# Kernel tuning notes

Hardware: AMD Instinct MI355X
Metric: run time of the kernel (lower is better)

Reference implementation:

```python
import jax, jax.numpy as jnp
import numpy as np

DIM = 300

def setup_inputs() -> dict:
    key = jax.random.key(0)
    k1, k2 = jax.random.split(key)
    article_concat = jax.random.normal(k1, (256, 2048, DIM), dtype=jnp.float32)
    options_concat = jax.random.normal(k2, (256, 64, DIM), dtype=jnp.float32)
    return {"article_concat": article_concat, "options_concat": options_concat}

def reference(article_concat, options_concat):
    # Mean-pool over the word dimension for both inputs, then concat features.
    article_mean = jnp.mean(article_concat, axis=1)   # [B, DIM]
    options_mean = jnp.mean(options_concat, axis=1)   # [B, DIM]
    return jnp.concatenate([article_mean, options_mean], axis=1)  # [B, 2*DIM]
```

## Files before the change

### kernel.cpp

```cpp
#include <hip/hip_runtime.h>


typedef float f4 __attribute__((ext_vector_type(4)));

#define B        256
#define DIM      300
#define J4       75
#define W_ART    2048
#define W_OPT    64
#define SPLIT    8
#define ROWS_PB  (W_ART / SPLIT)
#define ITERS    (ROWS_PB * J4 / DIM)

__global__ __launch_bounds__(DIM) void art_partial_kernel(
    const f4* __restrict__ art,
    f4* __restrict__ part)
{
    const int b = blockIdx.x;
    const int y = blockIdx.y;
    const int t = threadIdx.x;
    const int j = t % J4;

    const f4* p = art + (size_t)b * (W_ART * J4) + (size_t)y * (ROWS_PB * J4) + t;

    f4 a0 = {0.f, 0.f, 0.f, 0.f};
    f4 a1 = {0.f, 0.f, 0.f, 0.f};
    f4 a2 = {0.f, 0.f, 0.f, 0.f};
    f4 a3 = {0.f, 0.f, 0.f, 0.f};
    #pragma unroll 4
    for (int it = 0; it < ITERS; it += 4, p += 4 * DIM) {
        const f4 v0 = __builtin_nontemporal_load(&p[0 * DIM]);
        const f4 v1 = __builtin_nontemporal_load(&p[1 * DIM]);
        const f4 v2 = __builtin_nontemporal_load(&p[2 * DIM]);
        const f4 v3 = __builtin_nontemporal_load(&p[3 * DIM]);
        a0 += v0;
        a1 += v1;
        a2 += v2;
        a3 += v3;
    }
    a0 += a1;
    a2 += a3;
    a0 += a2;

    __shared__ f4 lds[DIM];
    lds[t] = a0;
    __syncthreads();
    if (t < J4) {
        const f4 r = lds[t] + lds[t + J4] + lds[t + 2 * J4] + lds[t + 3 * J4];
        part[((size_t)y * B + b) * J4 + j] = r;
    }
}

__global__ __launch_bounds__(DIM) void finalize_kernel(
    const float* __restrict__ part,
    const float* __restrict__ opt,
    float* __restrict__ out)
{
    const int b = blockIdx.x;
    const int c = threadIdx.x;

    float s = 0.f;
    #pragma unroll
    for (int y = 0; y < SPLIT; ++y)
        s += part[((size_t)y * B + b) * DIM + c];

    const float* ob = opt + (size_t)b * (W_OPT * DIM) + c;
    float o0 = 0.f, o1 = 0.f, o2 = 0.f, o3 = 0.f;
    #pragma unroll 4
    for (int w = 0; w < W_OPT; w += 4) {
        o0 += __builtin_nontemporal_load(&ob[(size_t)(w + 0) * DIM]);
        o1 += __builtin_nontemporal_load(&ob[(size_t)(w + 1) * DIM]);
        o2 += __builtin_nontemporal_load(&ob[(size_t)(w + 2) * DIM]);
        o3 += __builtin_nontemporal_load(&ob[(size_t)(w + 3) * DIM]);
    }

    float* ou = out + (size_t)b * (2 * DIM);
    ou[c]       = s * (1.0f / (float)W_ART);
    ou[DIM + c] = ((o0 + o1) + (o2 + o3)) * (1.0f / (float)W_OPT);
}

extern "C" void kernel_launch(void* const* d_in, const int* in_sizes, int n_in,
                              void* d_out, int out_size, void* d_ws, size_t ws_size,
                              hipStream_t stream) {
    const f4* art = (const f4*)d_in[0];
    const float* opt = (const float*)d_in[1];
    float* out = (float*)d_out;
    f4* part = (f4*)d_ws;

    art_partial_kernel<<<dim3(B, SPLIT), dim3(DIM), 0, stream>>>(art, part);
    finalize_kernel<<<dim3(B), dim3(DIM), 0, stream>>>((const float*)part, opt, out);
}
```

Before: 762.9 us.

## Fuse article and options mean into one kernel without split reduction

Replaces the two-kernel scheme (split partial sums over 8 blocks per batch, then a finalize kernel) with a single kernel of 600 threads per batch row that streams the whole article and options slabs and reduces through shared memory. This removes the second launch and the workspace round-trip, and drops the nontemporal load hints. The trade-off is fewer blocks (256 instead of 2048), which may limit memory-level parallelism on a 256-CU device.

```diff
diff --git a/kernel.cpp b/kernel.cpp
--- a/kernel.cpp
+++ b/kernel.cpp
@@ -8,85 +8,76 @@
 #define J4       75
 #define W_ART    2048
 #define W_OPT    64
-#define SPLIT    8
-#define ROWS_PB  (W_ART / SPLIT)
-#define ITERS    (ROWS_PB * J4 / DIM)
+#define THR      600
+#define GRP      (THR / J4)
+#define ART_F4   (W_ART * J4)
+#define ART_IT   (ART_F4 / THR)
+#define OPT_F4   (W_OPT * J4)
+#define OPT_IT   (OPT_F4 / THR)
 
-__global__ __launch_bounds__(DIM) void art_partial_kernel(
+__global__ __launch_bounds__(THR) void fused_mean_kernel(
     const f4* __restrict__ art,
-    f4* __restrict__ part)
+    const f4* __restrict__ opt,
+    f4* __restrict__ out)
 {
     const int b = blockIdx.x;
-    const int y = blockIdx.y;
     const int t = threadIdx.x;
-    const int j = t % J4;
 
-    const f4* p = art + (size_t)b * (W_ART * J4) + (size_t)y * (ROWS_PB * J4) + t;
-
+    const f4* pa = art + (size_t)b * ART_F4 + t;
     f4 a0 = {0.f, 0.f, 0.f, 0.f};
     f4 a1 = {0.f, 0.f, 0.f, 0.f};
     f4 a2 = {0.f, 0.f, 0.f, 0.f};
     f4 a3 = {0.f, 0.f, 0.f, 0.f};
     #pragma unroll 4
-    for (int it = 0; it < ITERS; it += 4, p += 4 * DIM) {
-        const f4 v0 = __builtin_nontemporal_load(&p[0 * DIM]);
-        const f4 v1 = __builtin_nontemporal_load(&p[1 * DIM]);
-        const f4 v2 = __builtin_nontemporal_load(&p[2 * DIM]);
-        const f4 v3 = __builtin_nontemporal_load(&p[3 * DIM]);
+    for (int it = 0; it < ART_IT; it += 4, pa += 4 * THR) {
+        const f4 v0 = pa[0 * THR];
+        const f4 v1 = pa[1 * THR];
+        const f4 v2 = pa[2 * THR];
+        const f4 v3 = pa[3 * THR];
         a0 += v0;
         a1 += v1;
         a2 += v2;
         a3 += v3;
     }
-    a0 += a1;
-    a2 += a3;
-    a0 += a2;
+    a0 += a1; a2 += a3; a0 += a2;
 
-    __shared__ f4 lds[DIM];
-    lds[t] = a0;
+    const f4* po = opt + (size_t)b * OPT_F4 + t;
+    f4 o0 = {0.f, 0.f, 0.f, 0.f};
+    f4 o1 = {0.f, 0.f, 0.f, 0.f};
+    #pragma unroll
+    for (int it = 0; it < OPT_IT; it += 2, po += 2 * THR) {
+        o0 += po[0];
+        o1 += po[THR];
+    }
+    o0 += o1;
+
+    __shared__ f4 lart[THR];
+    __shared__ f4 lopt[THR];
+    lart[t] = a0;
+    lopt[t] = o0;
     __syncthreads();
+
     if (t < J4) {
-        const f4 r = lds[t] + lds[t + J4] + lds[t + 2 * J4] + lds[t + 3 * J4];
-        part[((size_t)y * B + b) * J4 + j] = r;
+        f4 sa = lart[t];
+        f4 so = lopt[t];
+        #pragma unroll
+        for (int g = 1; g < GRP; ++g) {
+            sa += lart[t + g * J4];
+            so += lopt[t + g * J4];
+        }
+        f4* ou = out + (size_t)b * (2 * J4);
+        ou[t]      = sa * (1.0f / (float)W_ART);
+        ou[J4 + t] = so * (1.0f / (float)W_OPT);
     }
-}
-
-__global__ __launch_bounds__(DIM) void finalize_kernel(
-    const float* __restrict__ part,
-    const float* __restrict__ opt,
-    float* __restrict__ out)
-{
-    const int b = blockIdx.x;
-    const int c = threadIdx.x;
-
-    float s = 0.f;
-    #pragma unroll
-    for (int y = 0; y < SPLIT; ++y)
-        s += part[((size_t)y * B + b) * DIM + c];
-
-    const float* ob = opt + (size_t)b * (W_OPT * DIM) + c;
-    float o0 = 0.f, o1 = 0.f, o2 = 0.f, o3 = 0.f;
-    #pragma unroll 4
-    for (int w = 0; w < W_OPT; w += 4) {
-        o0 += __builtin_nontemporal_load(&ob[(size_t)(w + 0) * DIM]);
-        o1 += __builtin_nontemporal_load(&ob[(size_t)(w + 1) * DIM]);
-        o2 += __builtin_nontemporal_load(&ob[(size_t)(w + 2) * DIM]);
-        o3 += __builtin_nontemporal_load(&ob[(size_t)(w + 3) * DIM]);
-    }
-
-    float* ou = out + (size_t)b * (2 * DIM);
-    ou[c]       = s * (1.0f / (float)W_ART);
-    ou[DIM + c] = ((o0 + o1) + (o2 + o3)) * (1.0f / (float)W_OPT);
 }
 
 extern "C" void kernel_launch(void* const* d_in, const int* in_sizes, int n_in,
                               void* d_out, int out_size, void* d_ws, size_t ws_size,
                               hipStream_t stream) {
     const f4* art = (const f4*)d_in[0];
-    const float* opt = (const float*)d_in[1];
-    float* out = (float*)d_out;
-    f4* part = (f4*)d_ws;
+    const f4* opt = (const f4*)d_in[1];
+    f4* out = (f4*)d_out;
+    (void)d_ws; (void)ws_size;
 
-    art_partial_kernel<<<dim3(B, SPLIT), dim3(DIM), 0, stream>>>(art, part);
-    finalize_kernel<<<dim3(B), dim3(DIM), 0, stream>>>((const float*)part, opt, out);
+    fused_mean_kernel<<<dim3(B), dim3(THR), 0, stream>>>(art, opt, out);
 }
```

Measured after the change: 805.2 us. 5.5% more time.
